# Kernel optimization log

Hardware: AMD Instinct MI355X
Metric: run time of the kernel (lower is better)

## Reference

```python
import jax, jax.numpy as jnp
import numpy as np

NUM_HEADS_Q = 32
NUM_HEADS_KV = 8
HEAD_DIM = 128
THETA = 500000.0
B = 2
S = 1024


def _precompute_freqs(head_dim, seq_len, theta):
    half = head_dim // 2
    freqs = 1.0 / theta ** (jnp.arange(half, dtype=jnp.float32) / half)
    positions = jnp.arange(seq_len, dtype=jnp.float32)
    angles = positions[:, None] * freqs[None, :]  # (S, half)
    return jnp.cos(angles), jnp.sin(angles)


def _apply_rope(x, cos, sin):
    # x: (B, H, S, D); cos/sin: (S, D//2)
    half = x.shape[-1] // 2
    x1, x2 = x[..., :half], x[..., half:]
    c = cos[None, None]
    s = sin[None, None]
    return jnp.concatenate([x1 * c - x2 * s, x1 * s + x2 * c], axis=-1)


def setup_inputs() -> dict:
    key = jax.random.key(0)
    kq, kk, kv = jax.random.split(key, 3)
    q = jax.random.normal(kq, (B, 1, S, NUM_HEADS_Q * HEAD_DIM), dtype=jnp.float32)
    k = jax.random.normal(kk, (B, 1, S, NUM_HEADS_KV * HEAD_DIM), dtype=jnp.float32)
    v = jax.random.normal(kv, (B, 1, S, NUM_HEADS_KV * HEAD_DIM), dtype=jnp.float32)
    return {"q": q, "k": k, "v": v}


def reference(q, k, v) -> jnp.ndarray:
    D = HEAD_DIM
    gqa = NUM_HEADS_Q // NUM_HEADS_KV
    scale = 1.0 / np.sqrt(D).astype(np.float32)

    # (B,1,S,H*D) -> (B,H,S,D)
    qh = q.reshape(B, S, NUM_HEADS_Q, D).transpose(0, 2, 1, 3)
    kh = k.reshape(B, S, NUM_HEADS_KV, D).transpose(0, 2, 1, 3)
    vh = v.reshape(B, S, NUM_HEADS_KV, D).transpose(0, 2, 1, 3)

    cos, sin = _precompute_freqs(D, S, THETA)
    qh = _apply_rope(qh, cos, sin)
    kh = _apply_rope(kh, cos, sin)

    if gqa > 1:
        kh = jnp.repeat(kh, gqa, axis=1)   # (B, Hq, S, D)
        vh = jnp.repeat(vh, gqa, axis=1)

    scores = jnp.einsum('bhqd,bhkd->bhqk', qh, kh) * scale  # (B, Hq, S, S)
    causal = jnp.tril(jnp.ones((S, S), dtype=bool))
    scores = jnp.where(causal[None, None], scores, -jnp.inf)
    weights = jax.nn.softmax(scores, axis=-1)
    attn = jnp.einsum('bhqk,bhkd->bhqd', weights, vh)  # (B, Hq, S, D)
    out = attn.transpose(0, 2, 1, 3).reshape(B, 1, S, NUM_HEADS_Q * D)
    return out
```

## Files before the change

### kernel.cpp

```cpp
#include <hip/hip_runtime.h>
#include <math.h>

typedef __attribute__((ext_vector_type(4))) float f32x4;
typedef __attribute__((ext_vector_type(8))) short bf16x8;

namespace {
constexpr int kB = 2;
constexpr int kS = 1024;
constexpr int kD = 128;
constexpr int kQT = 64;
constexpr int kKT = 32;
constexpr int kNT = kS / kQT;
constexpr float kScale = 0.08838834764831845f;
constexpr float kLog2e = 1.4426950408889634f;
constexpr float kFreqC = 0.20503692777194262f;
constexpr int kKPad = 136;
constexpr int kVPad = 72;

constexpr size_t kTabOff = 0;
constexpr size_t kKOff = 512 * 1024;
constexpr size_t kVOff = kKOff + 4194304;
constexpr size_t kWsNeed = kVOff + 4194304;
}

#define VMCNT(n) asm volatile("s_waitcnt vmcnt(" #n ")" ::: "memory")

__device__ inline short f2bf(float f) {
  union { float f; unsigned u; } c{f};
  unsigned r = c.u + 0x7fffu + ((c.u >> 16) & 1u);
  return (short)(r >> 16);
}

__device__ inline unsigned pkbf(float a, float b) {
  unsigned r;
  asm("v_cvt_pk_bf16_f32 %0, %1, %2" : "=v"(r) : "v"(a), "v"(b));
  return r;
}

__device__ inline void gload16(const void* g, void* l) {
  __builtin_amdgcn_global_load_lds(
      (const __attribute__((address_space(1))) void*)g,
      (__attribute__((address_space(3))) void*)l, 16, 0, 0);
}

__global__ __launch_bounds__(256) void rope_table_k(float2* __restrict__ tab) {
  int t = blockIdx.x * 256 + threadIdx.x;
  int pos = t >> 6, j = t & 63;
  float ang = (float)pos * expf(-(float)j * kFreqC);
  float sn, cs;
  sincosf(ang, &sn, &cs);
  tab[t] = make_float2(cs, sn);
}

__global__ __launch_bounds__(256) void prep_k(
    const float* __restrict__ k, const float* __restrict__ v,
    const float2* __restrict__ tab, short* __restrict__ Kp,
    short* __restrict__ Vp) {
  __shared__ float Tl[64][68];
  int bid = blockIdx.x;
  if (bid < 1024) {
    int t2 = bid * 256 + threadIdx.x;
    int j = (t2 & 15) * 4;
    int h = (t2 >> 4) & 7;
    int s = (t2 >> 7) & 1023;
    int b = t2 >> 17;
    size_t sidx = ((size_t)b * 1024 + s) * 1024 + h * 128 + j;
    size_t didx = (((size_t)b * 8 + h) * 1024 + s) * 128 + j;
    float4 x1 = *(const float4*)&k[sidx];
    float4 x2 = *(const float4*)&k[sidx + 64];
    float4 t0 = *(const float4*)&tab[s * 64 + j];
    float4 t1 = *(const float4*)&tab[s * 64 + j + 2];
    short4 y1, y2;
    y1.x = f2bf(x1.x * t0.x - x2.x * t0.y);
    y2.x = f2bf(x1.x * t0.y + x2.x * t0.x);
    y1.y = f2bf(x1.y * t0.z - x2.y * t0.w);
    y2.y = f2bf(x1.y * t0.w + x2.y * t0.z);
    y1.z = f2bf(x1.z * t1.x - x2.z * t1.y);
    y2.z = f2bf(x1.z * t1.y + x2.z * t1.x);
    y1.w = f2bf(x1.w * t1.z - x2.w * t1.w);
    y2.w = f2bf(x1.w * t1.w + x2.w * t1.z);
    *(short4*)&Kp[didx] = y1;
    *(short4*)&Kp[didx + 64] = y2;
  } else {
    int blk = bid - 1024;
    int bh = blk >> 5;
    int rem = blk & 31;
    int s0 = (rem >> 1) * 64;
    int d0 = (rem & 1) * 64;
    int t = threadIdx.x;
#pragma unroll
    for (int i = 0; i < 4; ++i) {
      int srow = i * 16 + (t >> 4);
      int scol = (t & 15) * 4;
      float4 x = *(const float4*)&v[((size_t)(bh >> 3) * 1024 + s0 + srow) * 1024 +
                                    (bh & 7) * 128 + d0 + scol];
      *(float4*)&Tl[srow][scol] = x;
    }
    __syncthreads();
#pragma unroll
    for (int i = 0; i < 4; ++i) {
      int drow = i * 16 + (t >> 4);
      int sq = (t & 15) * 4;
      short4 y;
      y.x = f2bf(Tl[sq + 0][drow]);
      y.y = f2bf(Tl[sq + 1][drow]);
      y.z = f2bf(Tl[sq + 2][drow]);
      y.w = f2bf(Tl[sq + 3][drow]);
      *(short4*)&Vp[((size_t)bh * 128 + d0 + drow) * 1024 + s0 + sq] = y;
    }
  }
}

__global__ __launch_bounds__(256, 4) void attn_swp_k(
    const float* __restrict__ q, const short* __restrict__ Kp,
    const short* __restrict__ Vp, const float2* __restrict__ tab,
    float* __restrict__ out) {
  __shared__ char KV[2][16384];

  const int tid = threadIdx.x;
  const int w = tid >> 6;
  const int lane = tid & 63;
  const int lrow = lane & 15;
  const int hi = lane >> 4;
  const int lk8 = hi * 8;
  const int qt = ((int)blockIdx.x + 4 * (int)blockIdx.z +
                  8 * ((int)blockIdx.y >> 4)) & 15;
  const int hq = blockIdx.y;
  const int b = blockIdx.z;
  const int hkv = hq >> 2;
  const int q0 = qt * kQT;
  const int nk = 2 * (qt + 1);

  const char* Kh = (const char*)(Kp + ((size_t)b * 8 + hkv) * 1024 * 128);
  const char* Vh = (const char*)(Vp + ((size_t)b * 8 + hkv) * 128 * 1024);

#define STAGE32(k0_, dstbuf_)                                                 \
  {                                                                           \
    char* Kd = KV[dstbuf_];                                                   \
    _Pragma("unroll") for (int ii = 0; ii < 2; ++ii) {                        \
      int i = w * 2 + ii;                                                     \
      int row = i * 4 + hi;                                                   \
      int srcb = ((k0_) + row) * 256 + (((lane & 15) * 16) ^ ((row & 7) << 4)); \
      gload16(Kh + srcb, Kd + i * 1024);                                      \
    }                                                                         \
    _Pragma("unroll") for (int ii = 0; ii < 2; ++ii) {                        \
      int i = w * 2 + ii;                                                     \
      int vrow = i * 16 + (lane >> 2);                                        \
      int srcb = vrow * 2048 + (k0_) * 2 +                                    \
                 (((lane & 3) * 16) ^ (((vrow >> 1) & 3) << 4));              \
      gload16(Vh + srcb, Kd + 8192 + i * 1024);                               \
    }                                                                         \
  }

  const int pos = q0 + w * 16 + lrow;
  const float* qrow = q + ((size_t)b * 1024 + pos) * 4096 + hq * kD;
  const float2* tp = tab + (size_t)pos * 64;
  float4 x1a0 = *(const float4*)&qrow[lk8];
  float4 x1b0 = *(const float4*)&qrow[lk8 + 4];
  float4 x2a0 = *(const float4*)&qrow[lk8 + 64];
  float4 x2b0 = *(const float4*)&qrow[lk8 + 68];
  float4 x1a1 = *(const float4*)&qrow[32 + lk8];
  float4 x1b1 = *(const float4*)&qrow[32 + lk8 + 4];
  float4 x2a1 = *(const float4*)&qrow[32 + lk8 + 64];
  float4 x2b1 = *(const float4*)&qrow[32 + lk8 + 68];
  float4 ta0 = *(const float4*)&tp[lk8];
  float4 tb0 = *(const float4*)&tp[lk8 + 2];
  float4 tc0 = *(const float4*)&tp[lk8 + 4];
  float4 td0 = *(const float4*)&tp[lk8 + 6];
  float4 ta1 = *(const float4*)&tp[32 + lk8];
  float4 tb1 = *(const float4*)&tp[32 + lk8 + 2];
  float4 tc1 = *(const float4*)&tp[32 + lk8 + 4];
  float4 td1 = *(const float4*)&tp[32 + lk8 + 6];

  STAGE32(0, 0);

  bf16x8 qf[4];
  {
    bf16x8 lo, hb;
    lo[0] = f2bf((x1a0.x * ta0.x - x2a0.x * ta0.y) * kScale);
    hb[0] = f2bf((x1a0.x * ta0.y + x2a0.x * ta0.x) * kScale);
    lo[1] = f2bf((x1a0.y * ta0.z - x2a0.y * ta0.w) * kScale);
    hb[1] = f2bf((x1a0.y * ta0.w + x2a0.y * ta0.z) * kScale);
    lo[2] = f2bf((x1a0.z * tb0.x - x2a0.z * tb0.y) * kScale);
    hb[2] = f2bf((x1a0.z * tb0.y + x2a0.z * tb0.x) * kScale);
    lo[3] = f2bf((x1a0.w * tb0.z - x2a0.w * tb0.w) * kScale);
    hb[3] = f2bf((x1a0.w * tb0.w + x2a0.w * tb0.z) * kScale);
    lo[4] = f2bf((x1b0.x * tc0.x - x2b0.x * tc0.y) * kScale);
    hb[4] = f2bf((x1b0.x * tc0.y + x2b0.x * tc0.x) * kScale);
    lo[5] = f2bf((x1b0.y * tc0.z - x2b0.y * tc0.w) * kScale);
    hb[5] = f2bf((x1b0.y * tc0.w + x2b0.y * tc0.z) * kScale);
    lo[6] = f2bf((x1b0.z * td0.x - x2b0.z * td0.y) * kScale);
    hb[6] = f2bf((x1b0.z * td0.y + x2b0.z * td0.x) * kScale);
    lo[7] = f2bf((x1b0.w * td0.z - x2b0.w * td0.w) * kScale);
    hb[7] = f2bf((x1b0.w * td0.w + x2b0.w * td0.z) * kScale);
    qf[0] = lo; qf[2] = hb;
    lo[0] = f2bf((x1a1.x * ta1.x - x2a1.x * ta1.y) * kScale);
    hb[0] = f2bf((x1a1.x * ta1.y + x2a1.x * ta1.x) * kScale);
    lo[1] = f2bf((x1a1.y * ta1.z - x2a1.y * ta1.w) * kScale);
    hb[1] = f2bf((x1a1.y * ta1.w + x2a1.y * ta1.z) * kScale);
    lo[2] = f2bf((x1a1.z * tb1.x - x2a1.z * tb1.y) * kScale);
    hb[2] = f2bf((x1a1.z * tb1.y + x2a1.z * tb1.x) * kScale);
    lo[3] = f2bf((x1a1.w * tb1.z - x2a1.w * tb1.w) * kScale);
    hb[3] = f2bf((x1a1.w * tb1.w + x2a1.w * tb1.z) * kScale);
    lo[4] = f2bf((x1b1.x * tc1.x - x2b1.x * tc1.y) * kScale);
    hb[4] = f2bf((x1b1.x * tc1.y + x2b1.x * tc1.x) * kScale);
    lo[5] = f2bf((x1b1.y * tc1.z - x2b1.y * tc1.w) * kScale);
    hb[5] = f2bf((x1b1.y * tc1.w + x2b1.y * tc1.z) * kScale);
    lo[6] = f2bf((x1b1.z * td1.x - x2b1.z * td1.y) * kScale);
    hb[6] = f2bf((x1b1.z * td1.y + x2b1.z * td1.x) * kScale);
    lo[7] = f2bf((x1b1.w * td1.z - x2b1.w * td1.w) * kScale);
    hb[7] = f2bf((x1b1.w * td1.w + x2b1.w * td1.z) * kScale);
    qf[1] = lo; qf[3] = hb;
  }

  float m = -3e38f, l = 0.f;
  f32x4 acc[8];
#pragma unroll
  for (int dt = 0; dt < 8; ++dt) acc[dt] = f32x4{0.f, 0.f, 0.f, 0.f};

  const int srcA = lrow + 32 * (hi & 1);
  const int srcB = srcA + 16;
  const int c1 = hi >> 1;

  int buf = 0;
  for (int t = 0; t < nk; ++t) {
    const int k0 = t * kKT;
    if (t < nk - 1) {
      STAGE32((t + 1) * kKT, buf ^ 1);
      VMCNT(4);
    } else {
      VMCNT(0);
    }
    __builtin_amdgcn_sched_barrier(0);
    __builtin_amdgcn_s_barrier();
    __builtin_amdgcn_sched_barrier(0);

    const char* KsB = KV[buf];
    const char* VtB = KV[buf] + 8192;

    f32x4 sc[2];
    __builtin_amdgcn_s_setprio(1);
#pragma unroll
    for (int ct = 0; ct < 2; ++ct) {
      sc[ct] = f32x4{0.f, 0.f, 0.f, 0.f};
      int kr = ct * 16 + lrow;
#pragma unroll
      for (int d = 0; d < 4; ++d) {
        bf16x8 kf = *(const bf16x8*)(KsB + kr * 256 +
                                     ((d * 64 + hi * 16) ^ ((lrow & 7) << 4)));
        sc[ct] = __builtin_amdgcn_mfma_f32_16x16x32_bf16(kf, qf[d], sc[ct], 0, 0, 0);
      }
    }
    __builtin_amdgcn_s_setprio(0);

    if (t >= nk - 2) {
      int qg = q0 + w * 16 + lrow;
#pragma unroll
      for (int ct = 0; ct < 2; ++ct)
#pragma unroll
        for (int r = 0; r < 4; ++r)
          if (k0 + ct * 16 + hi * 4 + r > qg) sc[ct][r] = -3e38f;
    }

    float tv = fmaxf(fmaxf(fmaxf(sc[0][0], sc[0][1]), fmaxf(sc[0][2], sc[0][3])),
                     fmaxf(fmaxf(sc[1][0], sc[1][1]), fmaxf(sc[1][2], sc[1][3])));
    tv = fmaxf(tv, __shfl_xor(tv, 16));
    tv = fmaxf(tv, __shfl_xor(tv, 32));
    if (!__all(tv <= m + 8.f)) {
      float mn = fmaxf(m, tv);
      float al = exp2f((m - mn) * kLog2e);
      m = mn;
      l *= al;
      float alq[4];
#pragma unroll
      for (int r = 0; r < 4; ++r) alq[r] = __shfl(al, hi * 4 + r);
#pragma unroll
      for (int dt = 0; dt < 8; ++dt)
#pragma unroll
        for (int r = 0; r < 4; ++r) acc[dt][r] *= alq[r];
    }
    float p00 = exp2f((sc[0][0] - m) * kLog2e);
    float p01 = exp2f((sc[0][1] - m) * kLog2e);
    float p02 = exp2f((sc[0][2] - m) * kLog2e);
    float p03 = exp2f((sc[0][3] - m) * kLog2e);
    float p10 = exp2f((sc[1][0] - m) * kLog2e);
    float p11 = exp2f((sc[1][1] - m) * kLog2e);
    float p12 = exp2f((sc[1][2] - m) * kLog2e);
    float p13 = exp2f((sc[1][3] - m) * kLog2e);
    float rs = ((p00 + p01) + (p02 + p03)) + ((p10 + p11) + (p12 + p13));
    rs += __shfl_xor(rs, 16);
    rs += __shfl_xor(rs, 32);
    l += rs;

    unsigned u00 = pkbf(p00, p01), u01 = pkbf(p02, p03);
    unsigned u10 = pkbf(p10, p11), u11 = pkbf(p12, p13);
    unsigned A0 = (unsigned)__shfl((int)u00, srcA);
    unsigned A0b = (unsigned)__shfl((int)u10, srcA);
    unsigned A1 = (unsigned)__shfl((int)u01, srcA);
    unsigned A1b = (unsigned)__shfl((int)u11, srcA);
    unsigned B0 = (unsigned)__shfl((int)u00, srcB);
    unsigned B0b = (unsigned)__shfl((int)u10, srcB);
    unsigned B1 = (unsigned)__shfl((int)u01, srcB);
    unsigned B1b = (unsigned)__shfl((int)u11, srcB);
    union { unsigned u[4]; bf16x8 v; } pc;
    pc.u[0] = c1 ? A0b : A0;
    pc.u[1] = c1 ? A1b : A1;
    pc.u[2] = c1 ? B0b : B0;
    pc.u[3] = c1 ? B1b : B1;
    bf16x8 pa = pc.v;

    __builtin_amdgcn_s_setprio(1);
#pragma unroll
    for (int dt = 0; dt < 8; ++dt) {
      int rv = dt * 16 + lrow;
      bf16x8 vf = *(const bf16x8*)(VtB + rv * 64 +
                                   ((hi * 16) ^ (((rv >> 1) & 3) << 4)));
      acc[dt] = __builtin_amdgcn_mfma_f32_16x16x32_bf16(pa, vf, acc[dt], 0, 0, 0);
    }
    __builtin_amdgcn_s_setprio(0);
    __builtin_amdgcn_sched_barrier(0);
    __builtin_amdgcn_s_barrier();
    __builtin_amdgcn_sched_barrier(0);
    buf ^= 1;
  }

  float il[4];
#pragma unroll
  for (int r = 0; r < 4; ++r) il[r] = 1.f / __shfl(l, hi * 4 + r);
  float* ob = out + ((size_t)b * kS + q0 + w * 16) * 4096 + hq * kD;
#pragma unroll
  for (int dt = 0; dt < 8; ++dt)
#pragma unroll
    for (int r = 0; r < 4; ++r)
      ob[(hi * 4 + r) * 4096 + dt * 16 + lrow] = acc[dt][r] * il[r];
#undef STAGE32
}

template <bool USE_TAB>
__global__ __launch_bounds__(256) void attn_k(
    const float* __restrict__ q, const float* __restrict__ k,
    const float* __restrict__ v, const float2* __restrict__ tab,
    float* __restrict__ out) {
  __shared__ short Ksf[64][kKPad];
  __shared__ short Vtf[kD][kVPad];
  __shared__ short Qbuf[kQT * kKPad];
  const int tid = threadIdx.x;
  const int w = tid >> 6;
  const int lane = tid & 63;
  const int lrow = lane & 15;
  const int lk8 = (lane >> 4) * 8;
  const int qt = (int)gridDim.x - 1 - (int)blockIdx.x;
  const int hq = blockIdx.y;
  const int b = blockIdx.z;
  const int hkv = hq >> 2;
  const int q0 = qt * kQT;
  const float* qb = q + (size_t)b * kS * 4096 + hq * kD;
  const float* kb = k + (size_t)b * kS * 1024 + hkv * kD;
  const float* vb = v + (size_t)b * kS * 1024 + hkv * kD;
#pragma unroll
  for (int it = 0; it < 16; ++it) {
    int pi = tid + it * 256;
    int row = pi >> 6, j = pi & 63;
    int pos = q0 + row;
    float x1 = qb[(size_t)pos * 4096 + j];
    float x2 = qb[(size_t)pos * 4096 + j + 64];
    float c, s;
    if (USE_TAB) { float2 t2 = tab[(pos << 6) + j]; c = t2.x; s = t2.y; }
    else { float ang = (float)pos * __expf(-(float)j * kFreqC); __sincosf(ang, &s, &c); }
    Qbuf[row * kKPad + j]      = f2bf((x1 * c - x2 * s) * kScale);
    Qbuf[row * kKPad + j + 64] = f2bf((x1 * s + x2 * c) * kScale);
  }
  __syncthreads();
  bf16x8 qf[4];
#pragma unroll
  for (int d = 0; d < 4; ++d)
    qf[d] = *(const bf16x8*)&Qbuf[(w * 16 + lrow) * kKPad + d * 32 + lk8];
  __syncthreads();
  short* myP = Qbuf + w * 16 * kVPad;
  float mS[4] = {-3e38f, -3e38f, -3e38f, -3e38f};
  float lS[4] = {0.f, 0.f, 0.f, 0.f};
  f32x4 acc[8];
#pragma unroll
  for (int dt = 0; dt < 8; ++dt) acc[dt] = f32x4{0.f, 0.f, 0.f, 0.f};
  for (int kt = 0; kt <= qt; ++kt) {
    const int k0 = kt * 64;
#pragma unroll
    for (int it = 0; it < 16; ++it) {
      int pi = tid + it * 256;
      int row = pi >> 6, j = pi & 63;
      int pos = k0 + row;
      float x1 = kb[(size_t)pos * 1024 + j];
      float x2 = kb[(size_t)pos * 1024 + j + 64];
      float c, s;
      if (USE_TAB) { float2 t2 = tab[(pos << 6) + j]; c = t2.x; s = t2.y; }
      else { float ang = (float)pos * __expf(-(float)j * kFreqC); __sincosf(ang, &s, &c); }
      Ksf[row][j]      = f2bf(x1 * c - x2 * s);
      Ksf[row][j + 64] = f2bf(x1 * s + x2 * c);
    }
#pragma unroll
    for (int it = 0; it < 8; ++it) {
      int f = (tid + it * 256) * 4;
      int row = f >> 7, col = f & 127;
      const float4 v4 = *(const float4*)(vb + (size_t)(k0 + row) * 1024 + col);
      Vtf[col + 0][row] = f2bf(v4.x);
      Vtf[col + 1][row] = f2bf(v4.y);
      Vtf[col + 2][row] = f2bf(v4.z);
      Vtf[col + 3][row] = f2bf(v4.w);
    }
    __syncthreads();
    f32x4 sc[4];
#pragma unroll
    for (int ct = 0; ct < 4; ++ct) {
      sc[ct] = f32x4{0.f, 0.f, 0.f, 0.f};
#pragma unroll
      for (int d = 0; d < 4; ++d) {
        bf16x8 kf = *(const bf16x8*)&Ksf[ct * 16 + lrow][d * 32 + lk8];
        sc[ct] = __builtin_amdgcn_mfma_f32_16x16x32_bf16(qf[d], kf, sc[ct], 0, 0, 0);
      }
    }
    if (kt == qt) {
#pragma unroll
      for (int ct = 0; ct < 4; ++ct) {
        int col = ct * 16 + lrow;
#pragma unroll
        for (int r = 0; r < 4; ++r) {
          int row = w * 16 + (lane >> 4) * 4 + r;
          if (col > row) sc[ct][r] = -3e38f;
        }
      }
    }
#pragma unroll
    for (int r = 0; r < 4; ++r) {
      float t = fmaxf(fmaxf(sc[0][r], sc[1][r]), fmaxf(sc[2][r], sc[3][r]));
      t = fmaxf(t, __shfl_xor(t, 1));
      t = fmaxf(t, __shfl_xor(t, 2));
      t = fmaxf(t, __shfl_xor(t, 4));
      t = fmaxf(t, __shfl_xor(t, 8));
      float mn = fmaxf(mS[r], t);
      float al = exp2f((mS[r] - mn) * kLog2e);
      float rs = 0.f;
#pragma unroll
      for (int ct = 0; ct < 4; ++ct) {
        float p = exp2f((sc[ct][r] - mn) * kLog2e);
        sc[ct][r] = p;
        rs += p;
      }
      rs += __shfl_xor(rs, 1);
      rs += __shfl_xor(rs, 2);
      rs += __shfl_xor(rs, 4);
      rs += __shfl_xor(rs, 8);
      lS[r] = lS[r] * al + rs;
      mS[r] = mn;
#pragma unroll
      for (int dt = 0; dt < 8; ++dt) acc[dt][r] *= al;
    }
#pragma unroll
    for (int ct = 0; ct < 4; ++ct)
#pragma unroll
      for (int r = 0; r < 4; ++r)
        myP[((lane >> 4) * 4 + r) * kVPad + ct * 16 + lrow] = f2bf(sc[ct][r]);
#pragma unroll
    for (int ks = 0; ks < 2; ++ks) {
      bf16x8 pf = *(const bf16x8*)&myP[lrow * kVPad + ks * 32 + lk8];
#pragma unroll
      for (int dt = 0; dt < 8; ++dt) {
        bf16x8 vf = *(const bf16x8*)&Vtf[dt * 16 + lrow][ks * 32 + lk8];
        acc[dt] = __builtin_amdgcn_mfma_f32_16x16x32_bf16(pf, vf, acc[dt], 0, 0, 0);
      }
    }
    __syncthreads();
  }
  float il[4];
#pragma unroll
  for (int r = 0; r < 4; ++r) il[r] = 1.f / lS[r];
  float* ob = out + ((size_t)b * kS + q0 + w * 16) * 4096 + hq * kD;
#pragma unroll
  for (int dt = 0; dt < 8; ++dt)
#pragma unroll
    for (int r = 0; r < 4; ++r)
      ob[((lane >> 4) * 4 + r) * 4096 + dt * 16 + lrow] = acc[dt][r] * il[r];
}

extern "C" void kernel_launch(void* const* d_in, const int* in_sizes, int n_in,
                              void* d_out, int out_size, void* d_ws, size_t ws_size,
                              hipStream_t stream) {
  const float* q = (const float*)d_in[0];
  const float* k = (const float*)d_in[1];
  const float* v = (const float*)d_in[2];
  float* out = (float*)d_out;

  if (ws_size >= kWsNeed) {
    float2* tab = (float2*)((char*)d_ws + kTabOff);
    short* Kp = (short*)((char*)d_ws + kKOff);
    short* Vp = (short*)((char*)d_ws + kVOff);
    rope_table_k<<<256, 256, 0, stream>>>(tab);
    prep_k<<<1536, 256, 0, stream>>>(k, v, tab, Kp, Vp);
    dim3 grid(kNT, 32, kB);
    attn_swp_k<<<grid, 256, 0, stream>>>(q, Kp, Vp, tab, out);
  } else if (ws_size >= 512 * 1024) {
    float2* tab = (float2*)d_ws;
    rope_table_k<<<256, 256, 0, stream>>>(tab);
    dim3 grid(kNT, 32, kB);
    attn_k<true><<<grid, 256, 0, stream>>>(q, k, v, tab, out);
  } else {
    dim3 grid(kNT, 32, kB);
    attn_k<false><<<grid, 256, 0, stream>>>(q, k, v, nullptr, out);
  }
}
```

Baseline: 70.67 us.

## Switch attention to 32x32x16 MFMA with 128-row query tiles and 64-key blocks

Rewrites the main attention kernel to use 32x32x16 bf16 MFMA instead of 16x16x32. Each block now covers 128 query rows and each step 64 keys, with 32 KB double-buffered K/V stages. The P operand is built with v_permlane32_swap instead of many shuffles. The grid halves, and the q-tile mapping pairs batches in reverse order to balance causal work. The cost is higher register and LDS use per block (occupancy bound lowered to 2) and fewer, coarser blocks, which may hurt load balance.

```diff
diff --git a/kernel.cpp b/kernel.cpp
--- a/kernel.cpp
+++ b/kernel.cpp
@@ -2,15 +2,13 @@
 #include <math.h>
 
 typedef __attribute__((ext_vector_type(4))) float f32x4;
+typedef __attribute__((ext_vector_type(16))) float f32x16;
 typedef __attribute__((ext_vector_type(8))) short bf16x8;
 
 namespace {
 constexpr int kB = 2;
 constexpr int kS = 1024;
 constexpr int kD = 128;
-constexpr int kQT = 64;
-constexpr int kKT = 32;
-constexpr int kNT = kS / kQT;
 constexpr float kScale = 0.08838834764831845f;
 constexpr float kLog2e = 1.4426950408889634f;
 constexpr float kFreqC = 0.20503692777194262f;
@@ -111,123 +109,102 @@
   }
 }
 
-__global__ __launch_bounds__(256, 4) void attn_swp_k(
+__global__ __launch_bounds__(256, 2) void attn32_k(
     const float* __restrict__ q, const short* __restrict__ Kp,
     const short* __restrict__ Vp, const float2* __restrict__ tab,
     float* __restrict__ out) {
-  __shared__ char KV[2][16384];
+  __shared__ char KV[2][32768];
 
   const int tid = threadIdx.x;
   const int w = tid >> 6;
   const int lane = tid & 63;
-  const int lrow = lane & 15;
-  const int hi = lane >> 4;
-  const int lk8 = hi * 8;
-  const int qt = ((int)blockIdx.x + 4 * (int)blockIdx.z +
-                  8 * ((int)blockIdx.y >> 4)) & 15;
+  const int l31 = lane & 31;
+  const int hi5 = lane >> 5;
+  const int f = ((int)blockIdx.x + (int)blockIdx.y) & 7;
+  const int b = blockIdx.z;
+  const int qt = b ? (7 - f) : f;
   const int hq = blockIdx.y;
-  const int b = blockIdx.z;
   const int hkv = hq >> 2;
-  const int q0 = qt * kQT;
+  const int q0 = qt * 128;
   const int nk = 2 * (qt + 1);
 
   const char* Kh = (const char*)(Kp + ((size_t)b * 8 + hkv) * 1024 * 128);
   const char* Vh = (const char*)(Vp + ((size_t)b * 8 + hkv) * 128 * 1024);
 
-#define STAGE32(k0_, dstbuf_)                                                 \
+#define STAGE(k0_, bufi_)                                                     \
   {                                                                           \
-    char* Kd = KV[dstbuf_];                                                   \
-    _Pragma("unroll") for (int ii = 0; ii < 2; ++ii) {                        \
-      int i = w * 2 + ii;                                                     \
-      int row = i * 4 + hi;                                                   \
+    char* Kd = KV[bufi_];                                                     \
+    char* Vd = KV[bufi_] + 16384;                                             \
+    _Pragma("unroll") for (int ii = 0; ii < 4; ++ii) {                        \
+      int i = w * 4 + ii;                                                     \
+      int row = i * 4 + (lane >> 4);                                          \
       int srcb = ((k0_) + row) * 256 + (((lane & 15) * 16) ^ ((row & 7) << 4)); \
       gload16(Kh + srcb, Kd + i * 1024);                                      \
     }                                                                         \
-    _Pragma("unroll") for (int ii = 0; ii < 2; ++ii) {                        \
-      int i = w * 2 + ii;                                                     \
-      int vrow = i * 16 + (lane >> 2);                                        \
-      int srcb = vrow * 2048 + (k0_) * 2 +                                    \
-                 (((lane & 3) * 16) ^ (((vrow >> 1) & 3) << 4));              \
-      gload16(Vh + srcb, Kd + 8192 + i * 1024);                               \
+    _Pragma("unroll") for (int ii = 0; ii < 4; ++ii) {                        \
+      int i = w * 4 + ii;                                                     \
+      int d = i * 8 + (lane >> 3);                                            \
+      int srcb = d * 2048 + (k0_) * 2 + (((lane & 7) * 16) ^ ((d & 7) << 4)); \
+      gload16(Vh + srcb, Vd + i * 1024);                                      \
     }                                                                         \
   }
 
-  const int pos = q0 + w * 16 + lrow;
-  const float* qrow = q + ((size_t)b * 1024 + pos) * 4096 + hq * kD;
-  const float2* tp = tab + (size_t)pos * 64;
-  float4 x1a0 = *(const float4*)&qrow[lk8];
-  float4 x1b0 = *(const float4*)&qrow[lk8 + 4];
-  float4 x2a0 = *(const float4*)&qrow[lk8 + 64];
-  float4 x2b0 = *(const float4*)&qrow[lk8 + 68];
-  float4 x1a1 = *(const float4*)&qrow[32 + lk8];
-  float4 x1b1 = *(const float4*)&qrow[32 + lk8 + 4];
-  float4 x2a1 = *(const float4*)&qrow[32 + lk8 + 64];
-  float4 x2b1 = *(const float4*)&qrow[32 + lk8 + 68];
-  float4 ta0 = *(const float4*)&tp[lk8];
-  float4 tb0 = *(const float4*)&tp[lk8 + 2];
-  float4 tc0 = *(const float4*)&tp[lk8 + 4];
-  float4 td0 = *(const float4*)&tp[lk8 + 6];
-  float4 ta1 = *(const float4*)&tp[32 + lk8];
-  float4 tb1 = *(const float4*)&tp[32 + lk8 + 2];
-  float4 tc1 = *(const float4*)&tp[32 + lk8 + 4];
-  float4 td1 = *(const float4*)&tp[32 + lk8 + 6];
-
-  STAGE32(0, 0);
-
-  bf16x8 qf[4];
-  {
-    bf16x8 lo, hb;
-    lo[0] = f2bf((x1a0.x * ta0.x - x2a0.x * ta0.y) * kScale);
-    hb[0] = f2bf((x1a0.x * ta0.y + x2a0.x * ta0.x) * kScale);
-    lo[1] = f2bf((x1a0.y * ta0.z - x2a0.y * ta0.w) * kScale);
-    hb[1] = f2bf((x1a0.y * ta0.w + x2a0.y * ta0.z) * kScale);
-    lo[2] = f2bf((x1a0.z * tb0.x - x2a0.z * tb0.y) * kScale);
-    hb[2] = f2bf((x1a0.z * tb0.y + x2a0.z * tb0.x) * kScale);
-    lo[3] = f2bf((x1a0.w * tb0.z - x2a0.w * tb0.w) * kScale);
-    hb[3] = f2bf((x1a0.w * tb0.w + x2a0.w * tb0.z) * kScale);
-    lo[4] = f2bf((x1b0.x * tc0.x - x2b0.x * tc0.y) * kScale);
-    hb[4] = f2bf((x1b0.x * tc0.y + x2b0.x * tc0.x) * kScale);
-    lo[5] = f2bf((x1b0.y * tc0.z - x2b0.y * tc0.w) * kScale);
-    hb[5] = f2bf((x1b0.y * tc0.w + x2b0.y * tc0.z) * kScale);
-    lo[6] = f2bf((x1b0.z * td0.x - x2b0.z * td0.y) * kScale);
-    hb[6] = f2bf((x1b0.z * td0.y + x2b0.z * td0.x) * kScale);
-    lo[7] = f2bf((x1b0.w * td0.z - x2b0.w * td0.w) * kScale);
-    hb[7] = f2bf((x1b0.w * td0.w + x2b0.w * td0.z) * kScale);
-    qf[0] = lo; qf[2] = hb;
-    lo[0] = f2bf((x1a1.x * ta1.x - x2a1.x * ta1.y) * kScale);
-    hb[0] = f2bf((x1a1.x * ta1.y + x2a1.x * ta1.x) * kScale);
-    lo[1] = f2bf((x1a1.y * ta1.z - x2a1.y * ta1.w) * kScale);
-    hb[1] = f2bf((x1a1.y * ta1.w + x2a1.y * ta1.z) * kScale);
-    lo[2] = f2bf((x1a1.z * tb1.x - x2a1.z * tb1.y) * kScale);
-    hb[2] = f2bf((x1a1.z * tb1.y + x2a1.z * tb1.x) * kScale);
-    lo[3] = f2bf((x1a1.w * tb1.z - x2a1.w * tb1.w) * kScale);
-    hb[3] = f2bf((x1a1.w * tb1.w + x2a1.w * tb1.z) * kScale);
-    lo[4] = f2bf((x1b1.x * tc1.x - x2b1.x * tc1.y) * kScale);
-    hb[4] = f2bf((x1b1.x * tc1.y + x2b1.x * tc1.x) * kScale);
-    lo[5] = f2bf((x1b1.y * tc1.z - x2b1.y * tc1.w) * kScale);
-    hb[5] = f2bf((x1b1.y * tc1.w + x2b1.y * tc1.z) * kScale);
-    lo[6] = f2bf((x1b1.z * td1.x - x2b1.z * td1.y) * kScale);
-    hb[6] = f2bf((x1b1.z * td1.y + x2b1.z * td1.x) * kScale);
-    lo[7] = f2bf((x1b1.w * td1.z - x2b1.w * td1.w) * kScale);
-    hb[7] = f2bf((x1b1.w * td1.w + x2b1.w * td1.z) * kScale);
-    qf[1] = lo; qf[3] = hb;
+  STAGE(0, 0);
+
+  const int qrow = q0 + w * 32 + l31;
+  const float* qp = q + ((size_t)b * 1024 + qrow) * 4096 + hq * 128;
+  const float2* tp = tab + (size_t)qrow * 64;
+  bf16x8 qB[8];
+#pragma unroll
+  for (int g = 0; g < 4; ++g) {
+    int jb = g * 16 + hi5 * 8;
+    float4 x1a = *(const float4*)&qp[jb];
+    float4 x1b = *(const float4*)&qp[jb + 4];
+    float4 x2a = *(const float4*)&qp[jb + 64];
+    float4 x2b = *(const float4*)&qp[jb + 68];
+    float4 t0 = *(const float4*)&tp[jb];
+    float4 t1 = *(const float4*)&tp[jb + 2];
+    float4 t2 = *(const float4*)&tp[jb + 4];
+    float4 t3 = *(const float4*)&tp[jb + 6];
+    float lo[8], hb[8];
+    lo[0] = (x1a.x * t0.x - x2a.x * t0.y) * kScale;
+    hb[0] = (x1a.x * t0.y + x2a.x * t0.x) * kScale;
+    lo[1] = (x1a.y * t0.z - x2a.y * t0.w) * kScale;
+    hb[1] = (x1a.y * t0.w + x2a.y * t0.z) * kScale;
+    lo[2] = (x1a.z * t1.x - x2a.z * t1.y) * kScale;
+    hb[2] = (x1a.z * t1.y + x2a.z * t1.x) * kScale;
+    lo[3] = (x1a.w * t1.z - x2a.w * t1.w) * kScale;
+    hb[3] = (x1a.w * t1.w + x2a.w * t1.z) * kScale;
+    lo[4] = (x1b.x * t2.x - x2b.x * t2.y) * kScale;
+    hb[4] = (x1b.x * t2.y + x2b.x * t2.x) * kScale;
+    lo[5] = (x1b.y * t2.z - x2b.y * t2.w) * kScale;
+    hb[5] = (x1b.y * t2.w + x2b.y * t2.z) * kScale;
+    lo[6] = (x1b.z * t3.x - x2b.z * t3.y) * kScale;
+    hb[6] = (x1b.z * t3.y + x2b.z * t3.x) * kScale;
+    lo[7] = (x1b.w * t3.z - x2b.w * t3.w) * kScale;
+    hb[7] = (x1b.w * t3.w + x2b.w * t3.z) * kScale;
+    union { unsigned u[4]; bf16x8 v; } A, C;
+#pragma unroll
+    for (int ww = 0; ww < 4; ++ww) {
+      A.u[ww] = pkbf(lo[2 * ww], lo[2 * ww + 1]);
+      C.u[ww] = pkbf(hb[2 * ww], hb[2 * ww + 1]);
+    }
+    qB[g] = A.v;
+    qB[g + 4] = C.v;
   }
 
   float m = -3e38f, l = 0.f;
-  f32x4 acc[8];
-#pragma unroll
-  for (int dt = 0; dt < 8; ++dt) acc[dt] = f32x4{0.f, 0.f, 0.f, 0.f};
-
-  const int srcA = lrow + 32 * (hi & 1);
-  const int srcB = srcA + 16;
-  const int c1 = hi >> 1;
+  f32x16 acc[4];
+#pragma unroll
+  for (int dt = 0; dt < 4; ++dt)
+#pragma unroll
+    for (int e = 0; e < 16; ++e) acc[dt][e] = 0.f;
 
   int buf = 0;
   for (int t = 0; t < nk; ++t) {
-    const int k0 = t * kKT;
     if (t < nk - 1) {
-      STAGE32((t + 1) * kKT, buf ^ 1);
-      VMCNT(4);
+      STAGE((t + 1) * 64, buf ^ 1);
+      VMCNT(8);
     } else {
       VMCNT(0);
     }
@@ -235,105 +212,107 @@
     __builtin_amdgcn_s_barrier();
     __builtin_amdgcn_sched_barrier(0);
 
-    const char* KsB = KV[buf];
-    const char* VtB = KV[buf] + 8192;
-
-    f32x4 sc[2];
+    const char* Ks = KV[buf];
+    const char* Vt = KV[buf] + 16384;
+
+    f32x16 sc0, sc1;
+#pragma unroll
+    for (int e = 0; e < 16; ++e) { sc0[e] = 0.f; sc1[e] = 0.f; }
+    const int kswz = (l31 & 7) << 4;
     __builtin_amdgcn_s_setprio(1);
 #pragma unroll
-    for (int ct = 0; ct < 2; ++ct) {
-      sc[ct] = f32x4{0.f, 0.f, 0.f, 0.f};
-      int kr = ct * 16 + lrow;
-#pragma unroll
-      for (int d = 0; d < 4; ++d) {
-        bf16x8 kf = *(const bf16x8*)(KsB + kr * 256 +
-                                     ((d * 64 + hi * 16) ^ ((lrow & 7) << 4)));
-        sc[ct] = __builtin_amdgcn_mfma_f32_16x16x32_bf16(kf, qf[d], sc[ct], 0, 0, 0);
-      }
+    for (int c = 0; c < 8; ++c) {
+      int off = c * 32 + hi5 * 16;
+      bf16x8 k0f = *(const bf16x8*)(Ks + l31 * 256 + (off ^ kswz));
+      bf16x8 k1f = *(const bf16x8*)(Ks + (32 + l31) * 256 + (off ^ kswz));
+      sc0 = __builtin_amdgcn_mfma_f32_32x32x16_bf16(k0f, qB[c], sc0, 0, 0, 0);
+      sc1 = __builtin_amdgcn_mfma_f32_32x32x16_bf16(k1f, qB[c], sc1, 0, 0, 0);
     }
     __builtin_amdgcn_s_setprio(0);
 
-    if (t >= nk - 2) {
-      int qg = q0 + w * 16 + lrow;
-#pragma unroll
-      for (int ct = 0; ct < 2; ++ct)
-#pragma unroll
-        for (int r = 0; r < 4; ++r)
-          if (k0 + ct * 16 + hi * 4 + r > qg) sc[ct][r] = -3e38f;
-    }
-
-    float tv = fmaxf(fmaxf(fmaxf(sc[0][0], sc[0][1]), fmaxf(sc[0][2], sc[0][3])),
-                     fmaxf(fmaxf(sc[1][0], sc[1][1]), fmaxf(sc[1][2], sc[1][3])));
-    tv = fmaxf(tv, __shfl_xor(tv, 16));
+    if (64 * (t + 1) > q0 + 32 * w) {
+      int kb = t * 64 + hi5 * 4;
+#pragma unroll
+      for (int r = 0; r < 16; ++r) {
+        int off = (r & 3) + 8 * (r >> 2);
+        if (kb + off > qrow) sc0[r] = -3e38f;
+        if (kb + 32 + off > qrow) sc1[r] = -3e38f;
+      }
+    }
+
+    float tv = -3e38f;
+#pragma unroll
+    for (int r = 0; r < 16; ++r) tv = fmaxf(tv, fmaxf(sc0[r], sc1[r]));
     tv = fmaxf(tv, __shfl_xor(tv, 32));
     if (!__all(tv <= m + 8.f)) {
       float mn = fmaxf(m, tv);
       float al = exp2f((m - mn) * kLog2e);
       m = mn;
       l *= al;
-      float alq[4];
-#pragma unroll
-      for (int r = 0; r < 4; ++r) alq[r] = __shfl(al, hi * 4 + r);
-#pragma unroll
-      for (int dt = 0; dt < 8; ++dt)
-#pragma unroll
-        for (int r = 0; r < 4; ++r) acc[dt][r] *= alq[r];
-    }
-    float p00 = exp2f((sc[0][0] - m) * kLog2e);
-    float p01 = exp2f((sc[0][1] - m) * kLog2e);
-    float p02 = exp2f((sc[0][2] - m) * kLog2e);
-    float p03 = exp2f((sc[0][3] - m) * kLog2e);
-    float p10 = exp2f((sc[1][0] - m) * kLog2e);
-    float p11 = exp2f((sc[1][1] - m) * kLog2e);
-    float p12 = exp2f((sc[1][2] - m) * kLog2e);
-    float p13 = exp2f((sc[1][3] - m) * kLog2e);
-    float rs = ((p00 + p01) + (p02 + p03)) + ((p10 + p11) + (p12 + p13));
-    rs += __shfl_xor(rs, 16);
+#pragma unroll
+      for (int r = 0; r < 16; ++r) {
+        float alr = __shfl(al, (r & 3) + 8 * (r >> 2) + 4 * hi5);
+        acc[0][r] *= alr;
+        acc[1][r] *= alr;
+        acc[2][r] *= alr;
+        acc[3][r] *= alr;
+      }
+    }
+    float rs = 0.f;
+#pragma unroll
+    for (int r = 0; r < 16; ++r) {
+      sc0[r] = exp2f((sc0[r] - m) * kLog2e);
+      sc1[r] = exp2f((sc1[r] - m) * kLog2e);
+      rs += sc0[r] + sc1[r];
+    }
     rs += __shfl_xor(rs, 32);
     l += rs;
 
-    unsigned u00 = pkbf(p00, p01), u01 = pkbf(p02, p03);
-    unsigned u10 = pkbf(p10, p11), u11 = pkbf(p12, p13);
-    unsigned A0 = (unsigned)__shfl((int)u00, srcA);
-    unsigned A0b = (unsigned)__shfl((int)u10, srcA);
-    unsigned A1 = (unsigned)__shfl((int)u01, srcA);
-    unsigned A1b = (unsigned)__shfl((int)u11, srcA);
-    unsigned B0 = (unsigned)__shfl((int)u00, srcB);
-    unsigned B0b = (unsigned)__shfl((int)u10, srcB);
-    unsigned B1 = (unsigned)__shfl((int)u01, srcB);
-    unsigned B1b = (unsigned)__shfl((int)u11, srcB);
-    union { unsigned u[4]; bf16x8 v; } pc;
-    pc.u[0] = c1 ? A0b : A0;
-    pc.u[1] = c1 ? A1b : A1;
-    pc.u[2] = c1 ? B0b : B0;
-    pc.u[3] = c1 ? B1b : B1;
-    bf16x8 pa = pc.v;
-
     __builtin_amdgcn_s_setprio(1);
-#pragma unroll
-    for (int dt = 0; dt < 8; ++dt) {
-      int rv = dt * 16 + lrow;
-      bf16x8 vf = *(const bf16x8*)(VtB + rv * 64 +
-                                   ((hi * 16) ^ (((rv >> 1) & 3) << 4)));
-      acc[dt] = __builtin_amdgcn_mfma_f32_16x16x32_bf16(pa, vf, acc[dt], 0, 0, 0);
-    }
+#define PV_CHUNK(S, CI)                                                       \
+    {                                                                         \
+      unsigned p0 = pkbf(S[8 * ((CI) & 1) + 0], S[8 * ((CI) & 1) + 1]);       \
+      unsigned p1 = pkbf(S[8 * ((CI) & 1) + 2], S[8 * ((CI) & 1) + 3]);       \
+      unsigned p2 = pkbf(S[8 * ((CI) & 1) + 4], S[8 * ((CI) & 1) + 5]);       \
+      unsigned p3 = pkbf(S[8 * ((CI) & 1) + 6], S[8 * ((CI) & 1) + 7]);       \
+      asm("v_permlane32_swap_b32 %0, %1" : "+v"(p0), "+v"(p2));               \
+      asm("v_permlane32_swap_b32 %0, %1" : "+v"(p1), "+v"(p3));               \
+      union { unsigned u[4]; bf16x8 v; } pa;                                  \
+      pa.u[0] = p0; pa.u[1] = p1; pa.u[2] = p2; pa.u[3] = p3;                 \
+      int ko = (CI) * 32 + hi5 * 16;                                          \
+      _Pragma("unroll") for (int dt = 0; dt < 4; ++dt) {                      \
+        int d = dt * 32 + l31;                                                \
+        bf16x8 vf = *(const bf16x8*)(Vt + d * 128 + (ko ^ ((d & 7) << 4)));   \
+        acc[dt] =                                                             \
+            __builtin_amdgcn_mfma_f32_32x32x16_bf16(pa.v, vf, acc[dt], 0, 0, 0); \
+      }                                                                       \
+    }
+    PV_CHUNK(sc0, 0)
+    PV_CHUNK(sc0, 1)
+    PV_CHUNK(sc1, 2)
+    PV_CHUNK(sc1, 3)
+#undef PV_CHUNK
     __builtin_amdgcn_s_setprio(0);
+
     __builtin_amdgcn_sched_barrier(0);
     __builtin_amdgcn_s_barrier();
     __builtin_amdgcn_sched_barrier(0);
     buf ^= 1;
   }
 
-  float il[4];
-#pragma unroll
-  for (int r = 0; r < 4; ++r) il[r] = 1.f / __shfl(l, hi * 4 + r);
-  float* ob = out + ((size_t)b * kS + q0 + w * 16) * 4096 + hq * kD;
-#pragma unroll
-  for (int dt = 0; dt < 8; ++dt)
-#pragma unroll
-    for (int r = 0; r < 4; ++r)
-      ob[(hi * 4 + r) * 4096 + dt * 16 + lrow] = acc[dt][r] * il[r];
-#undef STAGE32
+  float linv = 1.f / l;
+  const size_t obase = ((size_t)b * 1024 + q0 + w * 32) * 4096 + (size_t)hq * 128;
+#pragma unroll
+  for (int r = 0; r < 16; ++r) {
+    int rq = (r & 3) + 8 * (r >> 2) + 4 * hi5;
+    float ilr = __shfl(linv, rq);
+    float* orow = out + obase + (size_t)rq * 4096 + l31;
+    orow[0]  = acc[0][r] * ilr;
+    orow[32] = acc[1][r] * ilr;
+    orow[64] = acc[2][r] * ilr;
+    orow[96] = acc[3][r] * ilr;
+  }
+#undef STAGE
 }
 
 template <bool USE_TAB>
@@ -343,7 +322,7 @@
     float* __restrict__ out) {
   __shared__ short Ksf[64][kKPad];
   __shared__ short Vtf[kD][kVPad];
-  __shared__ short Qbuf[kQT * kKPad];
+  __shared__ short Qbuf[64 * kKPad];
   const int tid = threadIdx.x;
   const int w = tid >> 6;
   const int lane = tid & 63;
@@ -353,7 +332,7 @@
   const int hq = blockIdx.y;
   const int b = blockIdx.z;
   const int hkv = hq >> 2;
-  const int q0 = qt * kQT;
+  const int q0 = qt * 64;
   const float* qb = q + (size_t)b * kS * 4096 + hq * kD;
   const float* kb = k + (size_t)b * kS * 1024 + hkv * kD;
   const float* vb = v + (size_t)b * kS * 1024 + hkv * kD;
@@ -495,15 +474,15 @@
     short* Vp = (short*)((char*)d_ws + kVOff);
     rope_table_k<<<256, 256, 0, stream>>>(tab);
     prep_k<<<1536, 256, 0, stream>>>(k, v, tab, Kp, Vp);
-    dim3 grid(kNT, 32, kB);
-    attn_swp_k<<<grid, 256, 0, stream>>>(q, Kp, Vp, tab, out);
+    dim3 grid(8, 32, kB);
+    attn32_k<<<grid, 256, 0, stream>>>(q, Kp, Vp, tab, out);
   } else if (ws_size >= 512 * 1024) {
     float2* tab = (float2*)d_ws;
     rope_table_k<<<256, 256, 0, stream>>>(tab);
-    dim3 grid(kNT, 32, kB);
+    dim3 grid(16, 32, kB);
     attn_k<true><<<grid, 256, 0, stream>>>(q, k, v, tab, out);
   } else {
-    dim3 grid(kNT, 32, kB);
+    dim3 grid(16, 32, kB);
     attn_k<false><<<grid, 256, 0, stream>>>(q, k, v, nullptr, out);
   }
 }
```

Result: faster. 64.15 us (-9.2%).
